# Performance work log

Hardware: AMD Instinct MI355X
Metric: run time of the kernel (lower is better)

The kernel has to match this reference:

```python
import jax, jax.numpy as jnp
import numpy as np

B, SQ, SE = 16, 1024, 1024
C_IN, C_ENC, DK, DV, H = 256, 256, 64, 64, 8
BN_EPS = 1e-5
NEG_SLOPE = 0.01  # torch LeakyReLU default


def setup_inputs() -> dict:
    key = jax.random.key(0)
    ks = jax.random.split(key, 8)
    x = jax.random.normal(ks[0], (B, SE, C_ENC), dtype=jnp.float32)
    q = jax.random.normal(ks[1], (B, SQ, C_IN), dtype=jnp.float32)
    # per-head 1x1-conv projection weights, stacked over heads
    Wq = jax.random.normal(ks[2], (H, DK, C_IN), dtype=jnp.float32) / np.sqrt(C_IN)
    Wk = jax.random.normal(ks[3], (H, DK, C_ENC), dtype=jnp.float32) / np.sqrt(C_ENC)
    Wv = jax.random.normal(ks[4], (H, DV, C_ENC), dtype=jnp.float32) / np.sqrt(C_ENC)
    # output projection (Conv1d(H*DV -> C_IN, k=1, bias=False))
    Wp = jax.random.normal(ks[5], (C_IN, H * DV), dtype=jnp.float32) / np.sqrt(H * DV)
    gamma = jax.random.normal(ks[6], (C_IN,), dtype=jnp.float32) * 0.1 + 1.0
    beta = jax.random.normal(ks[7], (C_IN,), dtype=jnp.float32) * 0.1
    return {"x": x, "q": q, "Wq": Wq, "Wk": Wk, "Wv": Wv, "Wp": Wp,
            "gamma": gamma, "beta": beta}


def reference(x, q, Wq, Wk, Wv, Wp, gamma, beta):
    # per-head Q/K/V via 1x1 conv == einsum over channel dim
    qh = jnp.einsum('bsc,hdc->bhsd', q, Wq)   # [B,H,SQ,DK]
    kh = jnp.einsum('btc,hdc->bhtd', x, Wk)   # [B,H,SE,DK]
    vh = jnp.einsum('btc,hec->bhte', x, Wv)   # [B,H,SE,DV]
    scale = 1.0 / jnp.sqrt(jnp.asarray(DK, dtype=qh.dtype))
    scores = jnp.einsum('bhsd,bhtd->bhst', qh, kh) * scale  # [B,H,SQ,SE]
    attn = jax.nn.softmax(scores, axis=-1)
    oh = jnp.einsum('bhst,bhte->bhse', attn, vh)  # [B,H,SQ,DV]
    # concat heads along feature dim (head-major order, as torch.cat over dim=2)
    o = jnp.transpose(oh, (0, 2, 1, 3)).reshape(B, SQ, H * DV)
    # LBRD projection: 1x1 conv -> BatchNorm1d (train mode: batch stats) -> LeakyReLU
    p = jnp.einsum('bsf,cf->bsc', o, Wp)  # [B,SQ,C_IN]
    mean = jnp.mean(p, axis=(0, 1))        # per-channel over (B, L)
    var = jnp.var(p, axis=(0, 1))          # biased, matching torch BN normalization
    y = (p - mean) * jax.lax.rsqrt(var + BN_EPS) * gamma + beta
    return jnp.where(y >= 0, y, NEG_SLOPE * y)
```

## Files before the change

kernel.cpp:

```cpp
#include <hip/hip_runtime.h>
#include <cstddef>

#define B_    16
#define SQ_   1024
#define SE_   1024
#define CIN_  256
#define DK_   64
#define H_    8
#define HD_   512
#define NROWS 16384
#define BN_EPS 1e-5f
#define NEG_SLOPE 0.01f

typedef __attribute__((ext_vector_type(8))) short bf16x8;
typedef __attribute__((ext_vector_type(4))) float f32x4;

#define BAR()        __builtin_amdgcn_s_barrier()
#define WAIT_LGKM0() asm volatile("s_waitcnt lgkmcnt(0)" ::: "memory")

__device__ __forceinline__ unsigned short f2bf(float f) {
    unsigned int u = __float_as_uint(f);
    return (unsigned short)((u + 0x7FFFu + ((u >> 16) & 1u)) >> 16);
}

#if __has_builtin(__builtin_amdgcn_perm)
__device__ __forceinline__ unsigned int pack_trunc(float lo, float hi) {
    return __builtin_amdgcn_perm(__float_as_uint(hi), __float_as_uint(lo), 0x07060302u);
}
#else
__device__ __forceinline__ unsigned int pack_trunc(float lo, float hi) {
    return (__float_as_uint(lo) >> 16) | (__float_as_uint(hi) & 0xFFFF0000u);
}
#endif

#if __has_builtin(__builtin_amdgcn_exp2f)
#define EXP2F(x) __builtin_amdgcn_exp2f(x)
#else
#define EXP2F(x) exp2f(x)
#endif

__device__ __forceinline__ ushort4 pack4(f32x4 v) {
    ushort4 p;
    p.x = f2bf(v[0]); p.y = f2bf(v[1]);
    p.z = f2bf(v[2]); p.w = f2bf(v[3]);
    return p;
}

__global__ __launch_bounds__(256) void wcast(const float* __restrict__ Wq,
                                             const float* __restrict__ Wk,
                                             const float* __restrict__ Wv,
                                             const float* __restrict__ Wp,
                                             unsigned short* __restrict__ dWq,
                                             unsigned short* __restrict__ dWkv,
                                             unsigned short* __restrict__ dWp,
                                             float* __restrict__ stats) {
    if (blockIdx.x < 2) stats[blockIdx.x * 256 + threadIdx.x] = 0.f;
    int i = blockIdx.x * 256 + threadIdx.x;
    int which = i >> 15, off = i & 32767;
    const float* s; unsigned short* d; float sc = 1.0f;
    if (which == 0)      { s = Wq; d = dWq; sc = 0.18033688011112042f; }
    else if (which == 1) { s = Wk; d = dWkv; }
    else if (which == 2) { s = Wv; d = dWkv + 131072; }
    else                 { s = Wp; d = dWp; }
    float4 v = *(const float4*)(s + (size_t)off * 4);
    ushort4 pk;
    pk.x = f2bf(v.x * sc); pk.y = f2bf(v.y * sc);
    pk.z = f2bf(v.z * sc); pk.w = f2bf(v.w * sc);
    *(ushort4*)(d + (size_t)off * 4) = pk;
}

__global__ __launch_bounds__(256) void gemm_qkv8(const float* __restrict__ qsrc,
                                                 const float* __restrict__ xsrc,
                                                 const unsigned short* __restrict__ Wqb,
                                                 const unsigned short* __restrict__ Wkvb,
                                                 unsigned short* __restrict__ qh,
                                                 unsigned short* __restrict__ khb,
                                                 unsigned short* __restrict__ vTb) {
    __shared__ __align__(16) unsigned short smem[18432];
    unsigned short* As = smem;
    unsigned short* Ws = smem + 9216;
    unsigned short* Cs = smem;

    const int tid = threadIdx.x;
    const int w = tid >> 6, l = tid & 63, lq = l >> 4, lr = l & 15;

    const int flat = blockIdx.x;
    const int xcd  = flat & 7;
    const int jj   = flat >> 3;
    const int bx   = jj % 12;
    const int by   = (jj / 12) + xcd * 16;

    const bool isQ = bx < 4;
    const bool isV = bx >= 8;
    const float* A = isQ ? qsrc : xsrc;
    const unsigned short* W = isQ ? Wqb : Wkvb;
    const int n0 = (isQ ? bx : bx - 4) * 128;
    const int m0 = by * 128;
    const int K = 256;

    const int srow = tid >> 1, soff = (tid & 1) * 32;

    f32x4 acc[2][8] = {};
    uint4 aR[8], wR[4];

    {
        const float* Ar = A + (size_t)(m0 + srow) * K + soff;
        #pragma unroll
        for (int c = 0; c < 8; ++c) aR[c] = *(const uint4*)(Ar + c * 4);
        const unsigned short* Wr = W + (size_t)(n0 + srow) * K + soff;
        #pragma unroll
        for (int c = 0; c < 4; ++c) wR[c] = *(const uint4*)(Wr + c * 8);
    }

    for (int k0 = 0; k0 < K; k0 += 64) {
        BAR();
        #pragma unroll
        for (int c = 0; c < 4; ++c) {
            float4 u0 = *(float4*)&aR[2 * c];
            float4 u1 = *(float4*)&aR[2 * c + 1];
            uint4 pk;
            pk.x = pack_trunc(u0.x, u0.y);
            pk.y = pack_trunc(u0.z, u0.w);
            pk.z = pack_trunc(u1.x, u1.y);
            pk.w = pack_trunc(u1.z, u1.w);
            *(uint4*)&As[srow * 72 + soff + c * 8] = pk;
            *(uint4*)&Ws[srow * 72 + soff + c * 8] = wR[c];
        }
        if (k0 + 64 < K) {
            const float* Ar = A + (size_t)(m0 + srow) * K + k0 + 64 + soff;
            #pragma unroll
            for (int c = 0; c < 8; ++c) aR[c] = *(const uint4*)(Ar + c * 4);
            const unsigned short* Wr = W + (size_t)(n0 + srow) * K + k0 + 64 + soff;
            #pragma unroll
            for (int c = 0; c < 4; ++c) wR[c] = *(const uint4*)(Wr + c * 8);
        }
        WAIT_LGKM0();
        BAR();

        if (!isV) {
            #pragma unroll
            for (int ks = 0; ks < 2; ++ks) {
                bf16x8 a0 = *(bf16x8*)&As[(w * 32 + lr) * 72 + ks * 32 + lq * 8];
                bf16x8 a1 = *(bf16x8*)&As[(w * 32 + 16 + lr) * 72 + ks * 32 + lq * 8];
                #pragma unroll
                for (int j = 0; j < 8; ++j) {
                    bf16x8 bb = *(bf16x8*)&Ws[(j * 16 + lr) * 72 + ks * 32 + lq * 8];
                    acc[0][j] = __builtin_amdgcn_mfma_f32_16x16x32_bf16(bb, a0, acc[0][j], 0, 0, 0);
                    acc[1][j] = __builtin_amdgcn_mfma_f32_16x16x32_bf16(bb, a1, acc[1][j], 0, 0, 0);
                }
            }
        } else {
            #pragma unroll
            for (int ks = 0; ks < 2; ++ks) {
                bf16x8 a0 = *(bf16x8*)&As[(w * 32 + lr) * 72 + ks * 32 + lq * 8];
                bf16x8 a1 = *(bf16x8*)&As[(w * 32 + 16 + lr) * 72 + ks * 32 + lq * 8];
                #pragma unroll
                for (int j = 0; j < 8; ++j) {
                    bf16x8 bb = *(bf16x8*)&Ws[(j * 16 + lr) * 72 + ks * 32 + lq * 8];
                    acc[0][j] = __builtin_amdgcn_mfma_f32_16x16x32_bf16(a0, bb, acc[0][j], 0, 0, 0);
                    acc[1][j] = __builtin_amdgcn_mfma_f32_16x16x32_bf16(a1, bb, acc[1][j], 0, 0, 0);
                }
            }
        }
    }

    __syncthreads();
    const int c16 = tid & 15;
    const int rb  = tid >> 4;
    if (!isV) {
        #pragma unroll
        for (int mf = 0; mf < 2; ++mf)
            #pragma unroll
            for (int j = 0; j < 8; ++j)
                *(ushort4*)&Cs[(w * 32 + mf * 16 + lr) * 144 + j * 16 + lq * 4] =
                    pack4(acc[mf][j]);
        __syncthreads();
        unsigned short* C = isQ ? qh : khb;
        #pragma unroll
        for (int it = 0; it < 8; ++it) {
            int r = it * 16 + rb;
            *(uint4*)(C + (size_t)(m0 + r) * 512 + n0 + c16 * 8) =
                *(const uint4*)(Cs + r * 144 + c16 * 8);
        }
    } else {
        #pragma unroll
        for (int mf = 0; mf < 2; ++mf)
            #pragma unroll
            for (int j = 0; j < 8; ++j)
                *(ushort4*)&Cs[(j * 16 + lr) * 144 + w * 32 + mf * 16 + lq * 4] =
                    pack4(acc[mf][j]);
        __syncthreads();
        const int bb = m0 >> 10, t0 = m0 & 1023;
        #pragma unroll
        for (int it = 0; it < 8; ++it) {
            int el = it * 16 + rb;
            int colv = n0 - 512 + el;
            int hh = colv >> 6, e = colv & 63;
            *(uint4*)(vTb + (size_t)((bb * 8 + hh) * 64 + e) * 1024 + t0 + c16 * 8) =
                *(const uint4*)(Cs + el * 144 + c16 * 8);
        }
    }
}

__global__ __launch_bounds__(256) void attn_mfma12(const unsigned short* __restrict__ qh,
                                                   const unsigned short* __restrict__ kh,
                                                   const unsigned short* __restrict__ vT,
                                                   unsigned short* __restrict__ o) {
    __shared__ __align__(16) unsigned short Ks[64 * 64];
    __shared__ __align__(16) unsigned short Vs[64 * 64];
    __shared__ __align__(16) unsigned short Ps[4][64 * 40];

    const int tid = threadIdx.x;
    const int w = tid >> 6, l = tid & 63, lq = l >> 4, lr = l & 15;

    const int flat = blockIdx.x;
    const int xcd  = flat & 7;
    const int jj   = flat >> 3;
    const int q0   = (jj & 3) * 256;
    const int hb   = (jj >> 2) + xcd * 16;
    const int h    = hb & 7;
    const int b    = hb >> 3;

    const int swz = (lr & 7) << 3;

    bf16x8 qf[4][2];
    #pragma unroll
    for (int mm = 0; mm < 4; ++mm) {
        const unsigned short* qr =
            qh + (size_t)(b * SQ_ + q0 + w * 64 + mm * 16 + lr) * HD_ + h * DK_;
        qf[mm][0] = *(const bf16x8*)(qr + lq * 8);
        qf[mm][1] = *(const bf16x8*)(qr + 32 + lq * 8);
    }

    const unsigned short* kb = kh + (size_t)(b * SE_) * HD_ + h * DK_;
    const unsigned short* vb = vT + (size_t)((b * 8 + h) * 64) * 1024;

    const int se = tid >> 3;
    const int sc = (tid & 7) * 8;
    const int sswz = (se & 7) << 3;

    float l_i[4] = {};
    f32x4 oacc[4][4] = {};
    unsigned short* Pw = Ps[w];

    uint4 kR[2], vR[2];
    #pragma unroll
    for (int ps = 0; ps < 2; ++ps) {
        int rr = se + ps * 32;
        kR[ps] = *(const uint4*)(kb + (size_t)rr * HD_ + sc);
        vR[ps] = *(const uint4*)(vb + (size_t)rr * 1024 + sc);
    }

    for (int t0 = 0; t0 < SE_; t0 += 64) {
        BAR();
        #pragma unroll
        for (int ps = 0; ps < 2; ++ps) {
            int rr = se + ps * 32;
            int ad = ((rr * 64 + sc) ^ sswz);
            *(uint4*)&Ks[ad] = kR[ps];
            *(uint4*)&Vs[ad] = vR[ps];
        }
        if (t0 + 64 < SE_) {
            #pragma unroll
            for (int ps = 0; ps < 2; ++ps) {
                int rr = se + ps * 32;
                kR[ps] = *(const uint4*)(kb + (size_t)(t0 + 64 + rr) * HD_ + sc);
                vR[ps] = *(const uint4*)(vb + (size_t)rr * 1024 + t0 + 64 + sc);
            }
        }
        WAIT_LGKM0();
        BAR();

        f32x4 s0[2][4] = {};
        __builtin_amdgcn_s_setprio(1);
        #pragma unroll
        for (int ks = 0; ks < 2; ++ks)
            #pragma unroll
            for (int tt = 0; tt < 2; ++tt) {
                bf16x8 kf = *(bf16x8*)&Ks[((tt * 16 + lr) * 64 + ks * 32 + lq * 8) ^ swz];
                #pragma unroll
                for (int mm = 0; mm < 4; ++mm)
                    s0[tt][mm] = __builtin_amdgcn_mfma_f32_16x16x32_bf16(kf, qf[mm][ks], s0[tt][mm], 0, 0, 0);
            }
        __builtin_amdgcn_s_setprio(0);

        #pragma unroll
        for (int mm = 0; mm < 4; ++mm)
            #pragma unroll
            for (int tt = 0; tt < 2; ++tt) {
                float e0 = EXP2F(s0[tt][mm][0]);
                float e1 = EXP2F(s0[tt][mm][1]);
                float e2 = EXP2F(s0[tt][mm][2]);
                float e3 = EXP2F(s0[tt][mm][3]);
                l_i[mm] += (e0 + e1) + (e2 + e3);
                uint2 pk;
                pk.x = pack_trunc(e0, e1);
                pk.y = pack_trunc(e2, e3);
                *(uint2*)&Pw[(mm * 16 + lr) * 40 + tt * 16 + lq * 4] = pk;
            }

        f32x4 s1[2][4] = {};
        __builtin_amdgcn_s_setprio(1);
        #pragma unroll
        for (int ks = 0; ks < 2; ++ks)
            #pragma unroll
            for (int tt = 0; tt < 2; ++tt) {
                bf16x8 kf = *(bf16x8*)&Ks[(((tt + 2) * 16 + lr) * 64 + ks * 32 + lq * 8) ^ swz];
                #pragma unroll
                for (int mm = 0; mm < 4; ++mm)
                    s1[tt][mm] = __builtin_amdgcn_mfma_f32_16x16x32_bf16(kf, qf[mm][ks], s1[tt][mm], 0, 0, 0);
            }
        __builtin_amdgcn_s_setprio(0);

        asm volatile("s_waitcnt lgkmcnt(0)" ::: "memory");

        __builtin_amdgcn_s_setprio(1);
        {
            bf16x8 pf[4];
            #pragma unroll
            for (int mm = 0; mm < 4; ++mm)
                pf[mm] = *(bf16x8*)&Pw[(mm * 16 + lr) * 40 + lq * 8];
            #pragma unroll
            for (int j = 0; j < 4; ++j) {
                bf16x8 vf = *(bf16x8*)&Vs[((j * 16 + lr) * 64 + lq * 8) ^ swz];
                #pragma unroll
                for (int mm = 0; mm < 4; ++mm)
                    oacc[mm][j] = __builtin_amdgcn_mfma_f32_16x16x32_bf16(vf, pf[mm], oacc[mm][j], 0, 0, 0);
            }
        }
        __builtin_amdgcn_s_setprio(0);

        #pragma unroll
        for (int mm = 0; mm < 4; ++mm)
            #pragma unroll
            for (int tt = 0; tt < 2; ++tt) {
                float e0 = EXP2F(s1[tt][mm][0]);
                float e1 = EXP2F(s1[tt][mm][1]);
                float e2 = EXP2F(s1[tt][mm][2]);
                float e3 = EXP2F(s1[tt][mm][3]);
                l_i[mm] += (e0 + e1) + (e2 + e3);
                uint2 pk;
                pk.x = pack_trunc(e0, e1);
                pk.y = pack_trunc(e2, e3);
                *(uint2*)&Pw[(mm * 16 + lr) * 40 + tt * 16 + lq * 4] = pk;
            }

        asm volatile("s_waitcnt lgkmcnt(0)" ::: "memory");

        __builtin_amdgcn_s_setprio(1);
        {
            bf16x8 pf[4];
            #pragma unroll
            for (int mm = 0; mm < 4; ++mm)
                pf[mm] = *(bf16x8*)&Pw[(mm * 16 + lr) * 40 + lq * 8];
            #pragma unroll
            for (int j = 0; j < 4; ++j) {
                bf16x8 vf = *(bf16x8*)&Vs[((j * 16 + lr) * 64 + 32 + lq * 8) ^ swz];
                #pragma unroll
                for (int mm = 0; mm < 4; ++mm)
                    oacc[mm][j] = __builtin_amdgcn_mfma_f32_16x16x32_bf16(vf, pf[mm], oacc[mm][j], 0, 0, 0);
            }
        }
        __builtin_amdgcn_s_setprio(0);
    }

    float inv[4];
    #pragma unroll
    for (int mm = 0; mm < 4; ++mm) {
        float t = l_i[mm];
        t += __shfl_xor(t, 16);
        t += __shfl_xor(t, 32);
        inv[mm] = 1.0f / t;
    }

    #pragma unroll
    for (int mm = 0; mm < 4; ++mm)
        #pragma unroll
        for (int j = 0; j < 4; ++j) {
            f32x4 v = oacc[mm][j];
            v[0] *= inv[mm]; v[1] *= inv[mm]; v[2] *= inv[mm]; v[3] *= inv[mm];
            *(ushort4*)&o[(size_t)(b * SQ_ + q0 + w * 64 + mm * 16 + lr) * HD_ +
                          h * DK_ + j * 16 + lq * 4] = pack4(v);
        }
}

__global__ __launch_bounds__(256) void gemm_out2(const unsigned short* __restrict__ A,
                                                 const unsigned short* __restrict__ W,
                                                 float* __restrict__ C,
                                                 float* __restrict__ gsum,
                                                 float* __restrict__ gsumsq) {
    __shared__ __align__(16) unsigned short As[128 * 72];
    __shared__ __align__(16) unsigned short Ws[64 * 72];
    const int tid = threadIdx.x;
    const int w = tid >> 6, l = tid & 63, lq = l >> 4, lr = l & 15;
    const int n0 = blockIdx.x * 64, m0 = blockIdx.y * 128;
    const int K = 512;

    const int arow = tid >> 1, aoff = (tid & 1) * 32;
    const int wrow = tid >> 2, woff = (tid & 3) * 16;

    f32x4 acc[2][4] = {};
    uint4 aR[4], wR[2];

    {
        const unsigned short* Ar = A + (size_t)(m0 + arow) * K + aoff;
        #pragma unroll
        for (int c = 0; c < 4; ++c) aR[c] = *(const uint4*)(Ar + c * 8);
        const unsigned short* Wr = W + (size_t)(n0 + wrow) * K + woff;
        #pragma unroll
        for (int c = 0; c < 2; ++c) wR[c] = *(const uint4*)(Wr + c * 8);
    }

    for (int k0 = 0; k0 < K; k0 += 64) {
        BAR();
        #pragma unroll
        for (int c = 0; c < 4; ++c)
            *(uint4*)&As[arow * 72 + aoff + c * 8] = aR[c];
        #pragma unroll
        for (int c = 0; c < 2; ++c)
            *(uint4*)&Ws[wrow * 72 + woff + c * 8] = wR[c];

        if (k0 + 64 < K) {
            const unsigned short* Ar = A + (size_t)(m0 + arow) * K + k0 + 64 + aoff;
            #pragma unroll
            for (int c = 0; c < 4; ++c) aR[c] = *(const uint4*)(Ar + c * 8);
            const unsigned short* Wr = W + (size_t)(n0 + wrow) * K + k0 + 64 + woff;
            #pragma unroll
            for (int c = 0; c < 2; ++c) wR[c] = *(const uint4*)(Wr + c * 8);
        }
        WAIT_LGKM0();
        BAR();

        #pragma unroll
        for (int ks = 0; ks < 2; ++ks) {
            bf16x8 a0 = *(bf16x8*)&As[(w * 32 + lr) * 72 + ks * 32 + lq * 8];
            bf16x8 a1 = *(bf16x8*)&As[(w * 32 + 16 + lr) * 72 + ks * 32 + lq * 8];
            #pragma unroll
            for (int j = 0; j < 4; ++j) {
                bf16x8 bb = *(bf16x8*)&Ws[(j * 16 + lr) * 72 + ks * 32 + lq * 8];
                acc[0][j] = __builtin_amdgcn_mfma_f32_16x16x32_bf16(a0, bb, acc[0][j], 0, 0, 0);
                acc[1][j] = __builtin_amdgcn_mfma_f32_16x16x32_bf16(a1, bb, acc[1][j], 0, 0, 0);
            }
        }
    }

    float cs[4] = {}, cq[4] = {};
    #pragma unroll
    for (int m = 0; m < 2; ++m)
        #pragma unroll
        for (int j = 0; j < 4; ++j)
            #pragma unroll
            for (int r = 0; r < 4; ++r) {
                float v = acc[m][j][r];
                C[(size_t)(m0 + w * 32 + m * 16 + lq * 4 + r) * 256 + n0 + j * 16 + lr] = v;
                cs[j] += v;
                cq[j] += v * v;
            }
    #pragma unroll
    for (int j = 0; j < 4; ++j) {
        cs[j] += __shfl_xor(cs[j], 16); cs[j] += __shfl_xor(cs[j], 32);
        cq[j] += __shfl_xor(cq[j], 16); cq[j] += __shfl_xor(cq[j], 32);
    }
    __syncthreads();
    float* red = (float*)As;
    if (lq == 0) {
        #pragma unroll
        for (int j = 0; j < 4; ++j) {
            red[w * 128 + j * 16 + lr]      = cs[j];
            red[w * 128 + 64 + j * 16 + lr] = cq[j];
        }
    }
    __syncthreads();
    if (tid < 128) {
        int col = tid & 63, stat = tid >> 6;
        float t = red[stat * 64 + col] + red[128 + stat * 64 + col] +
                  red[256 + stat * 64 + col] + red[384 + stat * 64 + col];
        atomicAdd((stat ? gsumsq : gsum) + n0 + col, t);
    }
}

__global__ __launch_bounds__(256) void bn_norm4(const float* __restrict__ p,
                                                const float* __restrict__ gsum,
                                                const float* __restrict__ gsumsq,
                                                const float* __restrict__ gamma,
                                                const float* __restrict__ beta,
                                                float* __restrict__ out) {
    int i = blockIdx.x * 256 + threadIdx.x;
    int c0 = (i * 4) & 255;
    const float invN = 1.0f / (float)NROWS;
    float4 pv = *(const float4*)(p + (size_t)i * 4);
    float vals[4] = {pv.x, pv.y, pv.z, pv.w};
    float res[4];
    #pragma unroll
    for (int k = 0; k < 4; ++k) {
        int c = c0 + k;
        float mean = gsum[c] * invN;
        float var  = gsumsq[c] * invN - mean * mean;
        float v = (vals[k] - mean) * rsqrtf(var + BN_EPS) * gamma[c] + beta[c];
        res[k] = v >= 0.f ? v : NEG_SLOPE * v;
    }
    float4 ov = {res[0], res[1], res[2], res[3]};
    *(float4*)(out + (size_t)i * 4) = ov;
}

extern "C" void kernel_launch(void* const* d_in, const int* in_sizes, int n_in,
                              void* d_out, int out_size, void* d_ws, size_t ws_size,
                              hipStream_t stream) {
    const float* x     = (const float*)d_in[0];
    const float* q     = (const float*)d_in[1];
    const float* Wq    = (const float*)d_in[2];
    const float* Wk    = (const float*)d_in[3];
    const float* Wv    = (const float*)d_in[4];
    const float* Wp    = (const float*)d_in[5];
    const float* gamma = (const float*)d_in[6];
    const float* beta  = (const float*)d_in[7];
    float* out = (float*)d_out;

    char* base = (char*)d_ws;
    unsigned short* Wqb  = (unsigned short*)(base + 0);
    unsigned short* Wkvb = (unsigned short*)(base + 262144);
    unsigned short* Wpb  = (unsigned short*)(base + 786432);
    unsigned short* qh   = (unsigned short*)(base + 1048576);
    unsigned short* khb  = (unsigned short*)(base + 17825792);
    unsigned short* vTb  = (unsigned short*)(base + 34603008);
    unsigned short* ob   = (unsigned short*)(base + 51380224);
    float*          pbuf = (float*)        (base + 68157440);
    float*          stats= (float*)        (base + 84934656);

    wcast<<<512, 256, 0, stream>>>(Wq, Wk, Wv, Wp, Wqb, Wkvb, Wpb, stats);

    gemm_qkv8<<<1536, 256, 0, stream>>>(q, x, Wqb, Wkvb, qh, khb, vTb);

    attn_mfma12<<<512, 256, 0, stream>>>(qh, khb, vTb, ob);

    gemm_out2<<<dim3(4, 128), 256, 0, stream>>>(ob, Wpb, pbuf, stats, stats + 256);

    bn_norm4<<<4096, 256, 0, stream>>>(pbuf, stats, stats + 256, gamma, beta, out);
}
```

Before: 227.0 us.

## Load A fragments directly to registers in QKV GEMM; halve attention query tile

The QKV projection kernel now stages the full 128x256 weight tile once in swizzled LDS. Each wave loads its own fp32 A rows straight into registers and converts them to bf16 MFMA fragments, with double-buffered prefetch across four k-steps. This removes the per-k-step A staging through LDS and the associated barriers, at the cost of more LDS per block (64KB) and possibly lower occupancy. Separately, the attention kernel uses 128-query tiles (32 rows per wave) instead of 256, doubling the grid to 1024 blocks for better occupancy and load balance. The trade-off is that K/V tiles are reloaded twice as often per query.

```diff
diff --git a/kernel.cpp b/kernel.cpp
--- a/kernel.cpp
+++ b/kernel.cpp
@@ -44,6 +44,15 @@
     p.x = f2bf(v[0]); p.y = f2bf(v[1]);
     p.z = f2bf(v[2]); p.w = f2bf(v[3]);
     return p;
+}
+
+__device__ __forceinline__ bf16x8 cvt8(float4 f0, float4 f1) {
+    uint4 pk;
+    pk.x = pack_trunc(f0.x, f0.y);
+    pk.y = pack_trunc(f0.z, f0.w);
+    pk.z = pack_trunc(f1.x, f1.y);
+    pk.w = pack_trunc(f1.z, f1.w);
+    return *(bf16x8*)&pk;
 }
 
 __global__ __launch_bounds__(256) void wcast(const float* __restrict__ Wq,
@@ -69,16 +78,15 @@
     *(ushort4*)(d + (size_t)off * 4) = pk;
 }
 
-__global__ __launch_bounds__(256) void gemm_qkv8(const float* __restrict__ qsrc,
+__global__ __launch_bounds__(256) void gemm_qkv9(const float* __restrict__ qsrc,
                                                  const float* __restrict__ xsrc,
                                                  const unsigned short* __restrict__ Wqb,
                                                  const unsigned short* __restrict__ Wkvb,
                                                  unsigned short* __restrict__ qh,
                                                  unsigned short* __restrict__ khb,
                                                  unsigned short* __restrict__ vTb) {
-    __shared__ __align__(16) unsigned short smem[18432];
-    unsigned short* As = smem;
-    unsigned short* Ws = smem + 9216;
+    __shared__ __align__(16) unsigned short smem[32768];
+    unsigned short* Ws = smem;
     unsigned short* Cs = smem;
 
     const int tid = threadIdx.x;
@@ -96,73 +104,70 @@
     const unsigned short* W = isQ ? Wqb : Wkvb;
     const int n0 = (isQ ? bx : bx - 4) * 128;
     const int m0 = by * 128;
-    const int K = 256;
-
-    const int srow = tid >> 1, soff = (tid & 1) * 32;
 
     f32x4 acc[2][8] = {};
-    uint4 aR[8], wR[4];
-
-    {
-        const float* Ar = A + (size_t)(m0 + srow) * K + soff;
-        #pragma unroll
-        for (int c = 0; c < 8; ++c) aR[c] = *(const uint4*)(Ar + c * 4);
-        const unsigned short* Wr = W + (size_t)(n0 + srow) * K + soff;
-        #pragma unroll
-        for (int c = 0; c < 4; ++c) wR[c] = *(const uint4*)(Wr + c * 8);
-    }
-
-    for (int k0 = 0; k0 < K; k0 += 64) {
-        BAR();
-        #pragma unroll
-        for (int c = 0; c < 4; ++c) {
-            float4 u0 = *(float4*)&aR[2 * c];
-            float4 u1 = *(float4*)&aR[2 * c + 1];
-            uint4 pk;
-            pk.x = pack_trunc(u0.x, u0.y);
-            pk.y = pack_trunc(u0.z, u0.w);
-            pk.z = pack_trunc(u1.x, u1.y);
-            pk.w = pack_trunc(u1.z, u1.w);
-            *(uint4*)&As[srow * 72 + soff + c * 8] = pk;
-            *(uint4*)&Ws[srow * 72 + soff + c * 8] = wR[c];
-        }
-        if (k0 + 64 < K) {
-            const float* Ar = A + (size_t)(m0 + srow) * K + k0 + 64 + soff;
-            #pragma unroll
-            for (int c = 0; c < 8; ++c) aR[c] = *(const uint4*)(Ar + c * 4);
-            const unsigned short* Wr = W + (size_t)(n0 + srow) * K + k0 + 64 + soff;
-            #pragma unroll
-            for (int c = 0; c < 4; ++c) wR[c] = *(const uint4*)(Wr + c * 8);
-        }
-        WAIT_LGKM0();
-        BAR();
-
-        if (!isV) {
-            #pragma unroll
-            for (int ks = 0; ks < 2; ++ks) {
-                bf16x8 a0 = *(bf16x8*)&As[(w * 32 + lr) * 72 + ks * 32 + lq * 8];
-                bf16x8 a1 = *(bf16x8*)&As[(w * 32 + 16 + lr) * 72 + ks * 32 + lq * 8];
-                #pragma unroll
-                for (int j = 0; j < 8; ++j) {
-                    bf16x8 bb = *(bf16x8*)&Ws[(j * 16 + lr) * 72 + ks * 32 + lq * 8];
-                    acc[0][j] = __builtin_amdgcn_mfma_f32_16x16x32_bf16(bb, a0, acc[0][j], 0, 0, 0);
-                    acc[1][j] = __builtin_amdgcn_mfma_f32_16x16x32_bf16(bb, a1, acc[1][j], 0, 0, 0);
-                }
-            }
-        } else {
-            #pragma unroll
-            for (int ks = 0; ks < 2; ++ks) {
-                bf16x8 a0 = *(bf16x8*)&As[(w * 32 + lr) * 72 + ks * 32 + lq * 8];
-                bf16x8 a1 = *(bf16x8*)&As[(w * 32 + 16 + lr) * 72 + ks * 32 + lq * 8];
-                #pragma unroll
-                for (int j = 0; j < 8; ++j) {
-                    bf16x8 bb = *(bf16x8*)&Ws[(j * 16 + lr) * 72 + ks * 32 + lq * 8];
-                    acc[0][j] = __builtin_amdgcn_mfma_f32_16x16x32_bf16(a0, bb, acc[0][j], 0, 0, 0);
-                    acc[1][j] = __builtin_amdgcn_mfma_f32_16x16x32_bf16(a1, bb, acc[1][j], 0, 0, 0);
-                }
-            }
-        }
-    }
+    float4 aA[8], aB[8];
+
+    const float* A0 = A + (size_t)(m0 + w * 32 + lr) * 256 + lq * 8;
+    const float* A1 = A + (size_t)(m0 + w * 32 + 16 + lr) * 256 + lq * 8;
+
+#define LOAD_A(buf, kstep) do {                                              \
+        buf[0] = *(const float4*)(A0 + (kstep) * 64);                        \
+        buf[1] = *(const float4*)(A0 + (kstep) * 64 + 4);                    \
+        buf[2] = *(const float4*)(A0 + (kstep) * 64 + 32);                   \
+        buf[3] = *(const float4*)(A0 + (kstep) * 64 + 36);                   \
+        buf[4] = *(const float4*)(A1 + (kstep) * 64);                        \
+        buf[5] = *(const float4*)(A1 + (kstep) * 64 + 4);                    \
+        buf[6] = *(const float4*)(A1 + (kstep) * 64 + 32);                   \
+        buf[7] = *(const float4*)(A1 + (kstep) * 64 + 36);                   \
+    } while (0)
+
+#define QKV_STEP(buf, kstep) do {                                            \
+        _Pragma("unroll")                                                    \
+        for (int ks = 0; ks < 2; ++ks) {                                     \
+            bf16x8 a0 = cvt8(buf[ks * 2], buf[ks * 2 + 1]);                  \
+            bf16x8 a1 = cvt8(buf[4 + ks * 2], buf[4 + ks * 2 + 1]);          \
+            const int colu = (kstep) * 8 + ks * 4 + lq;                      \
+            const int cswz = colu ^ (lr & 7);                                \
+            if (!isV) {                                                      \
+                _Pragma("unroll")                                            \
+                for (int j = 0; j < 8; ++j) {                                \
+                    bf16x8 bb = *(bf16x8*)&Ws[((j * 16 + lr) * 32 + cswz) * 8]; \
+                    acc[0][j] = __builtin_amdgcn_mfma_f32_16x16x32_bf16(bb, a0, acc[0][j], 0, 0, 0); \
+                    acc[1][j] = __builtin_amdgcn_mfma_f32_16x16x32_bf16(bb, a1, acc[1][j], 0, 0, 0); \
+                }                                                            \
+            } else {                                                         \
+                _Pragma("unroll")                                            \
+                for (int j = 0; j < 8; ++j) {                                \
+                    bf16x8 bb = *(bf16x8*)&Ws[((j * 16 + lr) * 32 + cswz) * 8]; \
+                    acc[0][j] = __builtin_amdgcn_mfma_f32_16x16x32_bf16(a0, bb, acc[0][j], 0, 0, 0); \
+                    acc[1][j] = __builtin_amdgcn_mfma_f32_16x16x32_bf16(a1, bb, acc[1][j], 0, 0, 0); \
+                }                                                            \
+            }                                                                \
+        }                                                                    \
+    } while (0)
+
+    LOAD_A(aA, 0);
+
+    #pragma unroll
+    for (int i = 0; i < 16; ++i) {
+        int u = tid + i * 256;
+        int row = u >> 5, colu = u & 31;
+        uint4 v = *(const uint4*)(W + (size_t)(n0 + row) * 256 + colu * 8);
+        *(uint4*)&Ws[(row * 32 + (colu ^ (row & 7))) * 8] = v;
+    }
+    __syncthreads();
+
+    LOAD_A(aB, 1);
+    QKV_STEP(aA, 0);
+    LOAD_A(aA, 2);
+    QKV_STEP(aB, 1);
+    LOAD_A(aB, 3);
+    QKV_STEP(aA, 2);
+    QKV_STEP(aB, 3);
+
+#undef LOAD_A
+#undef QKV_STEP
 
     __syncthreads();
     const int c16 = tid & 15;
@@ -202,13 +207,13 @@
     }
 }
 
-__global__ __launch_bounds__(256) void attn_mfma12(const unsigned short* __restrict__ qh,
+__global__ __launch_bounds__(256) void attn_mfma13(const unsigned short* __restrict__ qh,
                                                    const unsigned short* __restrict__ kh,
                                                    const unsigned short* __restrict__ vT,
                                                    unsigned short* __restrict__ o) {
     __shared__ __align__(16) unsigned short Ks[64 * 64];
     __shared__ __align__(16) unsigned short Vs[64 * 64];
-    __shared__ __align__(16) unsigned short Ps[4][64 * 40];
+    __shared__ __align__(16) unsigned short Ps[4][32 * 40];
 
     const int tid = threadIdx.x;
     const int w = tid >> 6, l = tid & 63, lq = l >> 4, lr = l & 15;
@@ -216,18 +221,18 @@
     const int flat = blockIdx.x;
     const int xcd  = flat & 7;
     const int jj   = flat >> 3;
-    const int q0   = (jj & 3) * 256;
-    const int hb   = (jj >> 2) + xcd * 16;
+    const int q0   = (jj & 7) * 128;
+    const int hb   = (jj >> 3) + xcd * 16;
     const int h    = hb & 7;
     const int b    = hb >> 3;
 
     const int swz = (lr & 7) << 3;
 
-    bf16x8 qf[4][2];
-    #pragma unroll
-    for (int mm = 0; mm < 4; ++mm) {
+    bf16x8 qf[2][2];
+    #pragma unroll
+    for (int mm = 0; mm < 2; ++mm) {
         const unsigned short* qr =
-            qh + (size_t)(b * SQ_ + q0 + w * 64 + mm * 16 + lr) * HD_ + h * DK_;
+            qh + (size_t)(b * SQ_ + q0 + w * 32 + mm * 16 + lr) * HD_ + h * DK_;
         qf[mm][0] = *(const bf16x8*)(qr + lq * 8);
         qf[mm][1] = *(const bf16x8*)(qr + 32 + lq * 8);
     }
@@ -239,8 +244,8 @@
     const int sc = (tid & 7) * 8;
     const int sswz = (se & 7) << 3;
 
-    float l_i[4] = {};
-    f32x4 oacc[4][4] = {};
+    float l_i[2] = {};
+    f32x4 oacc[2][4] = {};
     unsigned short* Pw = Ps[w];
 
     uint4 kR[2], vR[2];
@@ -271,7 +276,7 @@
         WAIT_LGKM0();
         BAR();
 
-        f32x4 s0[2][4] = {};
+        f32x4 s0[2][2] = {};
         __builtin_amdgcn_s_setprio(1);
         #pragma unroll
         for (int ks = 0; ks < 2; ++ks)
@@ -279,13 +284,13 @@
             for (int tt = 0; tt < 2; ++tt) {
                 bf16x8 kf = *(bf16x8*)&Ks[((tt * 16 + lr) * 64 + ks * 32 + lq * 8) ^ swz];
                 #pragma unroll
-                for (int mm = 0; mm < 4; ++mm)
+                for (int mm = 0; mm < 2; ++mm)
                     s0[tt][mm] = __builtin_amdgcn_mfma_f32_16x16x32_bf16(kf, qf[mm][ks], s0[tt][mm], 0, 0, 0);
             }
         __builtin_amdgcn_s_setprio(0);
 
         #pragma unroll
-        for (int mm = 0; mm < 4; ++mm)
+        for (int mm = 0; mm < 2; ++mm)
             #pragma unroll
             for (int tt = 0; tt < 2; ++tt) {
                 float e0 = EXP2F(s0[tt][mm][0]);
@@ -299,7 +304,7 @@
                 *(uint2*)&Pw[(mm * 16 + lr) * 40 + tt * 16 + lq * 4] = pk;
             }
 
-        f32x4 s1[2][4] = {};
+        f32x4 s1[2][2] = {};
         __builtin_amdgcn_s_setprio(1);
         #pragma unroll
         for (int ks = 0; ks < 2; ++ks)
@@ -307,7 +312,7 @@
             for (int tt = 0; tt < 2; ++tt) {
                 bf16x8 kf = *(bf16x8*)&Ks[(((tt + 2) * 16 + lr) * 64 + ks * 32 + lq * 8) ^ swz];
                 #pragma unroll
-                for (int mm = 0; mm < 4; ++mm)
+                for (int mm = 0; mm < 2; ++mm)
                     s1[tt][mm] = __builtin_amdgcn_mfma_f32_16x16x32_bf16(kf, qf[mm][ks], s1[tt][mm], 0, 0, 0);
             }
         __builtin_amdgcn_s_setprio(0);
@@ -316,22 +321,22 @@
 
         __builtin_amdgcn_s_setprio(1);
         {
-            bf16x8 pf[4];
-            #pragma unroll
-            for (int mm = 0; mm < 4; ++mm)
+            bf16x8 pf[2];
+            #pragma unroll
+            for (int mm = 0; mm < 2; ++mm)
                 pf[mm] = *(bf16x8*)&Pw[(mm * 16 + lr) * 40 + lq * 8];
             #pragma unroll
             for (int j = 0; j < 4; ++j) {
                 bf16x8 vf = *(bf16x8*)&Vs[((j * 16 + lr) * 64 + lq * 8) ^ swz];
                 #pragma unroll
-                for (int mm = 0; mm < 4; ++mm)
+                for (int mm = 0; mm < 2; ++mm)
                     oacc[mm][j] = __builtin_amdgcn_mfma_f32_16x16x32_bf16(vf, pf[mm], oacc[mm][j], 0, 0, 0);
             }
         }
         __builtin_amdgcn_s_setprio(0);
 
         #pragma unroll
-        for (int mm = 0; mm < 4; ++mm)
+        for (int mm = 0; mm < 2; ++mm)
             #pragma unroll
             for (int tt = 0; tt < 2; ++tt) {
                 float e0 = EXP2F(s1[tt][mm][0]);
@@ -349,24 +354,24 @@
 
         __builtin_amdgcn_s_setprio(1);
         {
-            bf16x8 pf[4];
-            #pragma unroll
-            for (int mm = 0; mm < 4; ++mm)
+            bf16x8 pf[2];
+            #pragma unroll
+            for (int mm = 0; mm < 2; ++mm)
                 pf[mm] = *(bf16x8*)&Pw[(mm * 16 + lr) * 40 + lq * 8];
             #pragma unroll
             for (int j = 0; j < 4; ++j) {
                 bf16x8 vf = *(bf16x8*)&Vs[((j * 16 + lr) * 64 + 32 + lq * 8) ^ swz];
                 #pragma unroll
-                for (int mm = 0; mm < 4; ++mm)
+                for (int mm = 0; mm < 2; ++mm)
                     oacc[mm][j] = __builtin_amdgcn_mfma_f32_16x16x32_bf16(vf, pf[mm], oacc[mm][j], 0, 0, 0);
             }
         }
         __builtin_amdgcn_s_setprio(0);
     }
 
-    float inv[4];
-    #pragma unroll
-    for (int mm = 0; mm < 4; ++mm) {
+    float inv[2];
+    #pragma unroll
+    for (int mm = 0; mm < 2; ++mm) {
         float t = l_i[mm];
         t += __shfl_xor(t, 16);
         t += __shfl_xor(t, 32);
@@ -374,12 +379,12 @@
     }
 
     #pragma unroll
-    for (int mm = 0; mm < 4; ++mm)
+    for (int mm = 0; mm < 2; ++mm)
         #pragma unroll
         for (int j = 0; j < 4; ++j) {
             f32x4 v = oacc[mm][j];
             v[0] *= inv[mm]; v[1] *= inv[mm]; v[2] *= inv[mm]; v[3] *= inv[mm];
-            *(ushort4*)&o[(size_t)(b * SQ_ + q0 + w * 64 + mm * 16 + lr) * HD_ +
+            *(ushort4*)&o[(size_t)(b * SQ_ + q0 + w * 32 + mm * 16 + lr) * HD_ +
                           h * DK_ + j * 16 + lq * 4] = pack4(v);
         }
 }
@@ -529,9 +534,9 @@
 
     wcast<<<512, 256, 0, stream>>>(Wq, Wk, Wv, Wp, Wqb, Wkvb, Wpb, stats);
 
-    gemm_qkv8<<<1536, 256, 0, stream>>>(q, x, Wqb, Wkvb, qh, khb, vTb);
-
-    attn_mfma12<<<512, 256, 0, stream>>>(qh, khb, vTb, ob);
+    gemm_qkv9<<<1536, 256, 0, stream>>>(q, x, Wqb, Wkvb, qh, khb, vTb);
+
+    attn_mfma13<<<1024, 256, 0, stream>>>(qh, khb, vTb, ob);
 
     gemm_out2<<<dim3(4, 128), 256, 0, stream>>>(ob, Wpb, pbuf, stats, stats + 256);
 
```

After: 224.4 us. No clear change (-1.1%).
